# Performance work log

Hardware: AMD Instinct MI355X
Metric: run time of the kernel (lower is better)

The kernel has to match this reference:

```python
import jax, jax.numpy as jnp
import numpy as np

B, N, D = 8, 1024, 1024
H, HD = 16, 64          # n_heads, head_dim = D // H
FF = 2 * D              # SwiGLU hidden dim (ffn_dim_mult=2)
EPS = 1e-5


def setup_inputs() -> dict:
    key = jax.random.key(0)
    ks = jax.random.split(key, 10)
    s = 0.02
    return {
        "x": jax.random.normal(ks[0], (B, N, D), dtype=jnp.float32),
        "attn_norm_scale": jnp.ones((D,), jnp.float32),
        "ffn_norm_scale": jnp.ones((D,), jnp.float32),
        "wq": jax.random.normal(ks[1], (D, D), jnp.float32) * s,
        "bq": jnp.zeros((D,), jnp.float32),
        "wk": jax.random.normal(ks[2], (D, D), jnp.float32) * s,
        "bk": jnp.zeros((D,), jnp.float32),
        "wv": jax.random.normal(ks[3], (D, D), jnp.float32) * s,
        "bv": jnp.zeros((D,), jnp.float32),
        "wo": jax.random.normal(ks[4], (D, D), jnp.float32) * s,
        "bo": jnp.zeros((D,), jnp.float32),
        "w_uv": jax.random.normal(ks[5], (D, 2 * FF), jnp.float32) * s,
        "w_out": jax.random.normal(ks[6], (FF, D), jnp.float32) * s,
    }


def _rmsnorm(x, scale):
    xf = x.astype(jnp.float32)
    y = xf * jax.lax.rsqrt(jnp.mean(xf * xf, axis=-1, keepdims=True) + EPS)
    return scale * y.astype(x.dtype)


def reference(x, attn_norm_scale, ffn_norm_scale, wq, bq, wk, bk, wv, bv,
              wo, bo, w_uv, w_out):
    # FFT2D: fft over channel dim then token dim, keep real part
    x = jnp.fft.fft(jnp.fft.fft(x, axis=-1), axis=-2).real.astype(jnp.float32)

    # --- self attention with pre-RMSNorm and residual ---
    xn = _rmsnorm(x, attn_norm_scale)
    q = (xn @ wq + bq).reshape(B, N, H, HD)
    k = (xn @ wk + bk).reshape(B, N, H, HD)
    v = (xn @ wv + bv).reshape(B, N, H, HD)
    scores = jnp.einsum('bnhd,bmhd->bhnm', q, k) / np.sqrt(HD).astype(np.float32)
    attn = jax.nn.softmax(scores, axis=-1)
    o = jnp.einsum('bhnm,bmhd->bnhd', attn, v).reshape(B, N, D)
    x = (o @ wo + bo) + x

    # --- SwiGLU FFN with pre-RMSNorm and residual ---
    xn = _rmsnorm(x, ffn_norm_scale)
    uv = xn @ w_uv                      # [B, N, 2*FF]
    u, vg = uv[..., :FF], uv[..., FF:]
    x = (jax.nn.silu(u) * vg) @ w_out + x
    return x
```

## Files before the change

kernel.cpp:

```cpp
#include <hip/hip_runtime.h>
#include <stdint.h>

typedef unsigned short u16;
typedef __attribute__((ext_vector_type(8))) __bf16 bf16x8;
typedef __attribute__((ext_vector_type(4))) float f32x4;
typedef __attribute__((ext_vector_type(8))) u16 u16x8;

static __device__ __forceinline__ u16 f2bf(float f){
  uint32_t x = __builtin_bit_cast(uint32_t, f);
  x = (x + 0x7FFFu + ((x >> 16) & 1u)) >> 16;
  return (u16)x;
}
static __device__ __forceinline__ u16 f2bf_fast(float f){
  uint32_t x = __builtin_bit_cast(uint32_t, f);
  return (u16)((x + 0x8000u) >> 16);
}
static __device__ __forceinline__ float bf2f(u16 h){
  uint32_t x = ((uint32_t)h) << 16;
  return __builtin_bit_cast(float, x);
}
static __device__ __forceinline__ f32x4 mfma16(bf16x8 a, bf16x8 b, f32x4 c){
  return __builtin_amdgcn_mfma_f32_16x16x32_bf16(a, b, c, 0, 0, 0);
}
static __device__ __forceinline__ void gload16(const void* g, void* l){
  __builtin_amdgcn_global_load_lds(
      (const __attribute__((address_space(1))) void*)(uintptr_t)g,
      (__attribute__((address_space(3))) void*)(uint32_t)(uintptr_t)l,
      16, 0, 0);
}

__global__ void k_tables(u16* __restrict__ C, u16* __restrict__ S){
  int n = blockIdx.x;
  int m0 = threadIdx.x * 4;
  #pragma unroll
  for (int i = 0; i < 4; ++i){
    int m = m0 + i;
    int ph = (n * m) & 1023;
    float a = (float)ph * (1.0f / 512.0f);
    int idx = n * 1024 + m;
    C[idx] = f2bf(cospif(a)); S[idx] = f2bf(sinpif(a));
  }
}

__global__ void k_tcvt(const float* __restrict__ in, u16* __restrict__ out,
                       int R, int Cc, int64_t inB, int64_t outB){
  __shared__ float t[32][33];
  const float* ip = in + (int64_t)blockIdx.z * inB;
  u16* op = out + (int64_t)blockIdx.z * outB;
  int tc = blockIdx.x * 32, tr = blockIdx.y * 32;
  int lx = threadIdx.x & 31, ly = threadIdx.x >> 5;
  #pragma unroll
  for (int i = 0; i < 32; i += 8)
    t[ly + i][lx] = ip[(int64_t)(tr + ly + i) * Cc + tc + lx];
  __syncthreads();
  #pragma unroll
  for (int i = 0; i < 32; i += 8)
    op[(int64_t)(tc + ly + i) * R + tr + lx] = f2bf(t[lx][ly + i]);
}

__global__ void k_tcvtW(const float* __restrict__ in, u16* __restrict__ out){
  __shared__ float t[32][33];
  int tc = blockIdx.x * 32, tr = blockIdx.y * 32;
  int lx = threadIdx.x & 31, ly = threadIdx.x >> 5;
  #pragma unroll
  for (int i = 0; i < 32; i += 8)
    t[ly + i][lx] = in[(int64_t)(tr + ly + i) * 4096 + tc + lx];
  __syncthreads();
  #pragma unroll
  for (int i = 0; i < 32; i += 8){
    int c = tc + ly + i;
    int pr = (c < 2048) ? ((c >> 4) * 32 + (c & 15))
                        : (((c - 2048) >> 4) * 32 + 16 + ((c - 2048) & 15));
    out[(int64_t)pr * 1024 + tr + lx] = f2bf(t[lx][ly + i]);
  }
}

__global__ void k_bias3(const float* __restrict__ a, const float* __restrict__ b,
                        const float* __restrict__ c, float* __restrict__ o){
  int i = blockIdx.x * 256 + threadIdx.x;
  o[i] = i < 1024 ? a[i] : (i < 2048 ? b[i - 1024] : c[i - 2048]);
}

__global__ __launch_bounds__(256) void k_rmsnorm(const float* __restrict__ x,
                                                 const float* __restrict__ sc,
                                                 u16* __restrict__ out){
  int r = blockIdx.x;
  const float4* px = (const float4*)(x + (int64_t)r * 1024);
  float4 v = px[threadIdx.x];
  float ss = v.x*v.x + v.y*v.y + v.z*v.z + v.w*v.w;
  #pragma unroll
  for (int o = 1; o < 64; o <<= 1) ss += __shfl_xor(ss, o);
  __shared__ float red[4];
  if ((threadIdx.x & 63) == 0) red[threadIdx.x >> 6] = ss;
  __syncthreads();
  float tot = red[0] + red[1] + red[2] + red[3];
  float rs = rsqrtf(tot * (1.0f / 1024.0f) + 1e-5f);
  float4 s4 = ((const float4*)sc)[threadIdx.x];
  ushort4 ov;
  ov.x = f2bf(v.x * rs * s4.x); ov.y = f2bf(v.y * rs * s4.y);
  ov.z = f2bf(v.z * rs * s4.z); ov.w = f2bf(v.w * rs * s4.w);
  ((ushort4*)(out + (int64_t)r * 1024))[threadIdx.x] = ov;
}

__global__ __launch_bounds__(256) void k_fftfin(const u16* __restrict__ Uw,
                                                const float* __restrict__ sc,
                                                float* __restrict__ Y,
                                                u16* __restrict__ xn){
  int row = blockIdx.x;
  int b = row >> 10, k = row & 1023;
  int kp = (k <= 512) ? k : 1024 - k;
  float sgn = (k <= 512) ? -1.0f : 1.0f;
  const u16* ub = Uw + (int64_t)b * (1280 * 1024) + (int64_t)kp * 1024;
  const u16* wb = ub + 640 * 1024;
  int c4 = threadIdx.x * 4;
  ushort4 uu = *(const ushort4*)(ub + c4);
  ushort4 ww = *(const ushort4*)(wb + c4);
  float y0 = bf2f(uu.x) + sgn * bf2f(ww.x);
  float y1 = bf2f(uu.y) + sgn * bf2f(ww.y);
  float y2 = bf2f(uu.z) + sgn * bf2f(ww.z);
  float y3 = bf2f(uu.w) + sgn * bf2f(ww.w);
  float ss = y0*y0 + y1*y1 + y2*y2 + y3*y3;
  #pragma unroll
  for (int o = 1; o < 64; o <<= 1) ss += __shfl_xor(ss, o);
  __shared__ float red[4];
  if ((threadIdx.x & 63) == 0) red[threadIdx.x >> 6] = ss;
  __syncthreads();
  float tot = red[0] + red[1] + red[2] + red[3];
  float rs = rsqrtf(tot * (1.0f / 1024.0f) + 1e-5f);
  float4 s4 = ((const float4*)sc)[threadIdx.x];
  float4 yo; yo.x = y0; yo.y = y1; yo.z = y2; yo.w = y3;
  ((float4*)(Y + (int64_t)row * 1024))[threadIdx.x] = yo;
  ushort4 ov;
  ov.x = f2bf(y0 * rs * s4.x); ov.y = f2bf(y1 * rs * s4.y);
  ov.z = f2bf(y2 * rs * s4.z); ov.w = f2bf(y3 * rs * s4.w);
  ((ushort4*)(xn + (int64_t)row * 1024))[threadIdx.x] = ov;
}


template<int BM, bool SILU>
__global__ __launch_bounds__(512, 2) void k_gemm3(
    const u16* __restrict__ A0, const u16* __restrict__ A1,
    const u16* __restrict__ B0, const u16* __restrict__ B1,
    void* Cout, const float* __restrict__ bias, const float* resid,
    int nkt, int rowSplit, int lda, int ldb, int ldc,
    int64_t aB, int64_t bB, int64_t cB, int outBf16)
{
  constexpr int MR = BM / 32;
  constexpr int ABUF = BM * 128;
  constexpr int BBUF = 32768;
  __shared__ char smem[2 * ABUF + 2 * BBUF];
  char* Abase = smem;
  char* Bbase = smem + 2 * ABUF;

  int z = blockIdx.z;
  int nwg = gridDim.x * gridDim.y;
  int bid = blockIdx.y * gridDim.x + blockIdx.x;
  int sw = (bid & 7) * (nwg >> 3) + (bid >> 3);
  int bx = sw % gridDim.x, by = sw / gridDim.x;

  int tm = by * BM, tn = bx * 256;
  int tid = threadIdx.x;
  int lane = tid & 63, w = tid >> 6;
  int lr = lane & 15, lg = lane >> 4;
  int wOffM = (w >> 2) * (MR * 16);
  int wOffN = (w & 3) * 64;

  const u16* Ap = ((tm < rowSplit) ? A0 : A1) + (int64_t)z * aB;
  const u16* Bp = ((tm < rowSplit) ? B0 : B1) + (int64_t)z * bB;
  int64_t cOff = (int64_t)z * cB;

  int sline = tid >> 3;
  int skg8 = (((tid & 7) ^ (sline & 7)) * 8);
  int64_t aAdr = (int64_t)(tm + sline) * lda + skg8;
  int64_t bAdr = (int64_t)(tn + sline) * ldb + skg8;

  int aRB = (wOffM + lr) * 128 + ((lg ^ (lr & 7)) * 16);
  int bRB = (wOffN + lr) * 128 + ((lg ^ (lr & 7)) * 16);

  auto stA = [&](int st, int h){
    char* d = Abase + (st & 1) * ABUF + h * 16384 + tid * 16;
    const u16* s = Ap + aAdr + (int64_t)(h * 128) * lda + st * 64;
    gload16(s, d);
    gload16(s + (int64_t)64 * lda, d + 8192);
  };
  auto stB = [&](int st, int h){
    char* d = Bbase + (st & 1) * BBUF + h * 16384 + tid * 16;
    const u16* s = Bp + bAdr + (int64_t)(h * 128) * ldb + st * 64;
    gload16(s, d);
    gload16(s + (int64_t)64 * ldb, d + 8192);
  };

  const f32x4 fz = {0.f, 0.f, 0.f, 0.f};
  f32x4 acc[MR][4];
  #pragma unroll
  for (int i = 0; i < MR; ++i)
    #pragma unroll
    for (int j = 0; j < 4; ++j) acc[i][j] = fz;

  stA(0, 0); if constexpr (BM == 256) stA(0, 1);
  stB(0, 0); stB(0, 1);
  stA(1, 0); if constexpr (BM == 256) stA(1, 1);
  stB(1, 0); stB(1, 1);
  if constexpr (BM == 256) asm volatile("s_waitcnt vmcnt(8)" ::: "memory");
  else                     asm volatile("s_waitcnt vmcnt(6)" ::: "memory");
  __builtin_amdgcn_s_barrier();

  for (int kt = 0; kt < nkt; ++kt){
    const char* Ab = Abase + (kt & 1) * ABUF;
    const char* Bb = Bbase + (kt & 1) * BBUF;
    int st = kt + 2;
    bool doSt = st < nkt;
    bf16x8 bl[2][2], bh[2][2];

    if constexpr (BM == 256){
      bf16x8 al[4][2], ah[4][2];
      #pragma unroll
      for (int i = 0; i < 4; ++i)
        #pragma unroll
        for (int kc = 0; kc < 2; ++kc)
          al[i][kc] = *(const bf16x8*)(Ab + ((aRB + i * 2048) ^ (kc << 6)));
      #pragma unroll
      for (int j = 0; j < 2; ++j)
        #pragma unroll
        for (int kc = 0; kc < 2; ++kc)
          bl[j][kc] = *(const bf16x8*)(Bb + ((bRB + j * 2048) ^ (kc << 6)));
      __builtin_amdgcn_s_barrier();
      __builtin_amdgcn_s_setprio(1);
      #pragma unroll
      for (int i = 0; i < 4; ++i)
        #pragma unroll
        for (int j = 0; j < 2; ++j)
          #pragma unroll
          for (int kc = 0; kc < 2; ++kc)
            acc[i][j] = mfma16(al[i][kc], bl[j][kc], acc[i][j]);
      __builtin_amdgcn_s_setprio(0);
      __builtin_amdgcn_s_barrier();
      #pragma unroll
      for (int j = 0; j < 2; ++j)
        #pragma unroll
        for (int kc = 0; kc < 2; ++kc)
          bh[j][kc] = *(const bf16x8*)(Bb + ((bRB + (j + 2) * 2048) ^ (kc << 6)));
      if (doSt){ stA(st, 0); stB(st, 0); }
      __builtin_amdgcn_s_barrier();
      __builtin_amdgcn_s_setprio(1);
      #pragma unroll
      for (int i = 0; i < 4; ++i)
        #pragma unroll
        for (int j = 0; j < 2; ++j)
          #pragma unroll
          for (int kc = 0; kc < 2; ++kc)
            acc[i][j + 2] = mfma16(al[i][kc], bh[j][kc], acc[i][j + 2]);
      __builtin_amdgcn_s_setprio(0);
      __builtin_amdgcn_s_barrier();
      #pragma unroll
      for (int i = 0; i < 4; ++i)
        #pragma unroll
        for (int kc = 0; kc < 2; ++kc)
          ah[i][kc] = *(const bf16x8*)(Ab + ((aRB + (i + 4) * 2048) ^ (kc << 6)));
      if (doSt) stB(st, 1);
      __builtin_amdgcn_s_barrier();
      __builtin_amdgcn_s_setprio(1);
      #pragma unroll
      for (int i = 0; i < 4; ++i)
        #pragma unroll
        for (int j = 0; j < 2; ++j)
          #pragma unroll
          for (int kc = 0; kc < 2; ++kc)
            acc[i + 4][j] = mfma16(ah[i][kc], bl[j][kc], acc[i + 4][j]);
      __builtin_amdgcn_s_setprio(0);
      __builtin_amdgcn_s_barrier();
      if (doSt) stA(st, 1);
      __builtin_amdgcn_s_barrier();
      __builtin_amdgcn_s_setprio(1);
      #pragma unroll
      for (int i = 0; i < 4; ++i)
        #pragma unroll
        for (int j = 0; j < 2; ++j)
          #pragma unroll
          for (int kc = 0; kc < 2; ++kc)
            acc[i + 4][j + 2] = mfma16(ah[i][kc], bh[j][kc], acc[i + 4][j + 2]);
      __builtin_amdgcn_s_setprio(0);
      if (doSt) asm volatile("s_waitcnt vmcnt(8)" ::: "memory");
      else      asm volatile("s_waitcnt vmcnt(0)" ::: "memory");
      __builtin_amdgcn_s_barrier();
    } else {
      bf16x8 al[4][2];
      #pragma unroll
      for (int i = 0; i < 4; ++i)
        #pragma unroll
        for (int kc = 0; kc < 2; ++kc)
          al[i][kc] = *(const bf16x8*)(Ab + ((aRB + i * 2048) ^ (kc << 6)));
      #pragma unroll
      for (int j = 0; j < 2; ++j)
        #pragma unroll
        for (int kc = 0; kc < 2; ++kc)
          bl[j][kc] = *(const bf16x8*)(Bb + ((bRB + j * 2048) ^ (kc << 6)));
      __builtin_amdgcn_s_barrier();
      __builtin_amdgcn_s_setprio(1);
      #pragma unroll
      for (int i = 0; i < 4; ++i)
        #pragma unroll
        for (int j = 0; j < 2; ++j)
          #pragma unroll
          for (int kc = 0; kc < 2; ++kc)
            acc[i][j] = mfma16(al[i][kc], bl[j][kc], acc[i][j]);
      __builtin_amdgcn_s_setprio(0);
      __builtin_amdgcn_s_barrier();
      #pragma unroll
      for (int j = 0; j < 2; ++j)
        #pragma unroll
        for (int kc = 0; kc < 2; ++kc)
          bh[j][kc] = *(const bf16x8*)(Bb + ((bRB + (j + 2) * 2048) ^ (kc << 6)));
      if (doSt){ stA(st, 0); stB(st, 0); stB(st, 1); }
      __builtin_amdgcn_s_barrier();
      __builtin_amdgcn_s_setprio(1);
      #pragma unroll
      for (int i = 0; i < 4; ++i)
        #pragma unroll
        for (int j = 0; j < 2; ++j)
          #pragma unroll
          for (int kc = 0; kc < 2; ++kc)
            acc[i][j + 2] = mfma16(al[i][kc], bh[j][kc], acc[i][j + 2]);
      __builtin_amdgcn_s_setprio(0);
      if (doSt) asm volatile("s_waitcnt vmcnt(6)" ::: "memory");
      else      asm volatile("s_waitcnt vmcnt(0)" ::: "memory");
      __builtin_amdgcn_s_barrier();
    }
  }

  if constexpr (SILU){
    #pragma unroll
    for (int i = 0; i < MR; ++i){
      int colBase = ((tn + wOffN) >> 1) + lr;
      #pragma unroll
      for (int jj = 0; jj < 4; ++jj){
        int row = tm + wOffM + i * 16 + lg * 4 + jj;
        #pragma unroll
        for (int jp = 0; jp < 2; ++jp){
          float u = acc[i][jp * 2][jj], v = acc[i][jp * 2 + 1][jj];
          float s = u / (1.0f + __expf(-u));
          ((u16*)Cout)[(int64_t)row * ldc + colBase + jp * 16] = f2bf(s * v);
        }
      }
    }
  } else {
    #pragma unroll
    for (int i = 0; i < MR; ++i){
      #pragma unroll
      for (int j = 0; j < 4; ++j){
        int col = tn + wOffN + j * 16 + lr;
        float badd = bias ? bias[col] : 0.0f;
        #pragma unroll
        for (int jj = 0; jj < 4; ++jj){
          int row = tm + wOffM + i * 16 + lg * 4 + jj;
          int64_t idx = cOff + (int64_t)row * ldc + col;
          float v = acc[i][j][jj] + badd;
          if (resid) v += resid[idx];
          if (outBf16) ((u16*)Cout)[idx] = f2bf(v);
          else         ((float*)Cout)[idx] = v;
        }
      }
    }
  }
}

__global__ __launch_bounds__(256) void k_vtrans(const u16* __restrict__ qkv,
                                                u16* __restrict__ vt){
  __shared__ u16 T[64 * 65];
  int bh = blockIdx.y; int b = bh >> 4, h = bh & 15;
  int kt = blockIdx.x;
  int t = threadIdx.x;
  const u16* src = qkv + (int64_t)(b * 1024 + kt * 64) * 3072 + 2048 + h * 64;
  #pragma unroll
  for (int i = 0; i < 16; ++i){
    int idx = i * 256 + t;
    int r = idx >> 6, c = idx & 63;
    T[r * 65 + c] = src[(int64_t)r * 3072 + c];
  }
  __syncthreads();
  u16* dst = vt + (int64_t)bh * 65536 + kt * 64;
  #pragma unroll
  for (int i = 0; i < 16; ++i){
    int idx = i * 256 + t;
    int dr = idx >> 6, kc = idx & 63;
    dst[(int64_t)dr * 1024 + kc] = T[kc * 65 + dr];
  }
}

__global__ __launch_bounds__(256, 3) void k_attn2(const u16* __restrict__ qkv,
                                                  const u16* __restrict__ vt,
                                                  u16* __restrict__ O){
  __shared__ u16 Ks[2][4096];
  __shared__ u16 Vts[2][4096];
  __shared__ u16 Pl[4][2304];
  int bh = blockIdx.y; int b = bh >> 4, h = bh & 15;
  int qt = blockIdx.x;
  int t = threadIdx.x, w = t >> 6, lane = t & 63, lr = lane & 15, lg = lane >> 4;
  int sr = t >> 3, sl = t & 7;
  int swz = (sl ^ (sr & 7)) * 8;

  const u16* kg = qkv + (int64_t)b * 1024 * 3072 + 1024 + h * 64;
  const u16* vg = vt + (int64_t)bh * 65536;

  const u16* qrow = qkv + (int64_t)(b * 1024 + qt * 128 + w * 32 + lr) * 3072 + h * 64;
  bf16x8 aq[2][2];
  #pragma unroll
  for (int m = 0; m < 2; ++m)
    #pragma unroll
    for (int kc = 0; kc < 2; ++kc)
      aq[m][kc] = *(const bf16x8*)(qrow + (int64_t)m * 16 * 3072 + kc * 32 + lg * 8);

  const f32x4 fz = {0.f, 0.f, 0.f, 0.f};
  f32x4 o_[2][4];
  float lj[2][4];
  #pragma unroll
  for (int m = 0; m < 2; ++m){
    #pragma unroll
    for (int d = 0; d < 4; ++d) o_[m][d] = fz;
    #pragma unroll
    for (int j = 0; j < 4; ++j) lj[m][j] = 0.f;
  }

  #define STAGE(ktile, bn) do {                                                   \
    int r0 = sr, r1 = 32 + sr;                                                    \
    gload16(kg + (int64_t)((ktile) * 64 + r0) * 3072 + swz,                       \
            (char*)Ks + (bn) * 8192 + (t >> 6) * 1024);                           \
    gload16(kg + (int64_t)((ktile) * 64 + r1) * 3072 + swz,                       \
            (char*)Ks + (bn) * 8192 + 4096 + (t >> 6) * 1024);                    \
    gload16(vg + (int64_t)r0 * 1024 + (ktile) * 64 + swz,                         \
            (char*)Vts + (bn) * 8192 + (t >> 6) * 1024);                          \
    gload16(vg + (int64_t)r1 * 1024 + (ktile) * 64 + swz,                         \
            (char*)Vts + (bn) * 8192 + 4096 + (t >> 6) * 1024);                   \
  } while (0)

  STAGE(0, 0);
  __syncthreads();
  int buf = 0;
  int lsw = lr & 7;

  const float CSC = 0.1803368801111204f;
  const float MSH = 8.656170245333781f;

  #pragma unroll 1
  for (int kt = 0; kt < 16; ++kt){
    if (kt < 15) STAGE(kt + 1, buf ^ 1);

    f32x4 s[2][4];
    #pragma unroll
    for (int m = 0; m < 2; ++m)
      #pragma unroll
      for (int n = 0; n < 4; ++n) s[m][n] = fz;
    #pragma unroll
    for (int n = 0; n < 4; ++n){
      #pragma unroll
      for (int kc = 0; kc < 2; ++kc){
        bf16x8 kb = *(const bf16x8*)&Ks[buf][(n * 16 + lr) * 64 + (((kc * 4 + lg) ^ lsw) * 8)];
        s[0][n] = mfma16(aq[0][kc], kb, s[0][n]);
        s[1][n] = mfma16(aq[1][kc], kb, s[1][n]);
      }
    }

    #pragma unroll
    for (int m = 0; m < 2; ++m){
      #pragma unroll
      for (int j = 0; j < 4; ++j){
        float p0 = exp2f(fmaf(s[m][0][j], CSC, -MSH));
        float p1 = exp2f(fmaf(s[m][1][j], CSC, -MSH));
        float p2 = exp2f(fmaf(s[m][2][j], CSC, -MSH));
        float p3 = exp2f(fmaf(s[m][3][j], CSC, -MSH));
        lj[m][j] += (p0 + p1) + (p2 + p3);
        u16* pb = &Pl[w][(m * 16 + lg * 4 + j) * 72 + lr];
        pb[0]  = f2bf_fast(p0); pb[16] = f2bf_fast(p1);
        pb[32] = f2bf_fast(p2); pb[48] = f2bf_fast(p3);
      }
    }
    asm volatile("s_waitcnt lgkmcnt(0)" ::: "memory");
    __builtin_amdgcn_sched_barrier(0);

    #pragma unroll
    for (int kc = 0; kc < 2; ++kc){
      bf16x8 pa0 = *(const bf16x8*)&Pl[w][(lr) * 72 + kc * 32 + lg * 8];
      bf16x8 pa1 = *(const bf16x8*)&Pl[w][(16 + lr) * 72 + kc * 32 + lg * 8];
      #pragma unroll
      for (int dt = 0; dt < 4; ++dt){
        bf16x8 vb = *(const bf16x8*)&Vts[buf][(dt * 16 + lr) * 64 + (((kc * 4 + lg) ^ lsw) * 8)];
        o_[0][dt] = mfma16(pa0, vb, o_[0][dt]);
        o_[1][dt] = mfma16(pa1, vb, o_[1][dt]);
      }
    }
    __syncthreads();
    buf ^= 1;
  }
  #undef STAGE

  u16* obase = O + (int64_t)(b * 1024 + qt * 128 + w * 32) * 1024 + h * 64;
  #pragma unroll
  for (int m = 0; m < 2; ++m){
    #pragma unroll
    for (int j = 0; j < 4; ++j){
      float l = lj[m][j];
      l += __shfl_xor(l, 1); l += __shfl_xor(l, 2);
      l += __shfl_xor(l, 4); l += __shfl_xor(l, 8);
      float inv = 1.0f / l;
      int q = m * 16 + lg * 4 + j;
      #pragma unroll
      for (int dt = 0; dt < 4; ++dt)
        obase[(int64_t)q * 1024 + dt * 16 + lr] = f2bf(o_[m][dt][j] * inv);
    }
  }
}

extern "C" void kernel_launch(void* const* d_in, const int* in_sizes, int n_in,
                              void* d_out, int out_size, void* d_ws, size_t ws_size,
                              hipStream_t stream)
{
  (void)in_sizes; (void)n_in; (void)out_size; (void)ws_size;
  const float* x    = (const float*)d_in[0];
  const float* ans  = (const float*)d_in[1];
  const float* fns  = (const float*)d_in[2];
  const float* wq   = (const float*)d_in[3];
  const float* bq   = (const float*)d_in[4];
  const float* wk   = (const float*)d_in[5];
  const float* bk   = (const float*)d_in[6];
  const float* wv   = (const float*)d_in[7];
  const float* bvv  = (const float*)d_in[8];
  const float* wo   = (const float*)d_in[9];
  const float* bo   = (const float*)d_in[10];
  const float* wuv  = (const float*)d_in[11];
  const float* wout = (const float*)d_in[12];

  char* ws = (char*)d_ws;
  const size_t MB = 1u << 20;
  const int64_t M1 = 1024 * 1024;
  const int64_t FB = (int64_t)1280 * 1024;
  const int BIG = 1 << 30;
  u16*  xbt   = (u16*)(ws + 0 * MB);
  u16*  Xcs   = (u16*)(ws + 16 * MB);
  u16*  Uw    = (u16*)(ws + 36 * MB);
  u16*  xn    = (u16*)(ws + 56 * MB);
  u16*  qkv   = (u16*)(ws + 0 * MB);
  u16*  vtg   = (u16*)(ws + 72 * MB);
  u16*  Obuf  = (u16*)(ws + 88 * MB);
  u16*  xn2   = (u16*)(ws + 0 * MB);
  u16*  g     = (u16*)(ws + 16 * MB);
  u16*  Cb    = (u16*)(ws + 104 * MB);
  u16*  Sb    = (u16*)(ws + 106 * MB);
  u16*  wqkvt = (u16*)(ws + 108 * MB);
  u16*  wot   = (u16*)(ws + 114 * MB);
  u16*  wuvt  = (u16*)(ws + 116 * MB);
  u16*  woutt = (u16*)(ws + 124 * MB);
  float* bqkv = (float*)(ws + 128 * MB);
  float* outF = (float*)d_out;

  k_tables<<<dim3(1024), 256, 0, stream>>>(Cb, Sb);
  k_tcvt<<<dim3(32, 32, 8), 256, 0, stream>>>(x, xbt, 1024, 1024, M1, M1);
  k_tcvt<<<dim3(32, 32, 1), 256, 0, stream>>>(wq, wqkvt,          1024, 1024, 0, 0);
  k_tcvt<<<dim3(32, 32, 1), 256, 0, stream>>>(wk, wqkvt + M1,     1024, 1024, 0, 0);
  k_tcvt<<<dim3(32, 32, 1), 256, 0, stream>>>(wv, wqkvt + 2 * M1, 1024, 1024, 0, 0);
  k_tcvt<<<dim3(32, 32, 1), 256, 0, stream>>>(wo, wot, 1024, 1024, 0, 0);
  k_tcvtW<<<dim3(128, 32), 256, 0, stream>>>(wuv, wuvt);
  k_tcvt<<<dim3(32, 64, 1), 256, 0, stream>>>(wout, woutt, 2048, 1024, 0, 0);
  k_bias3<<<dim3(12), 256, 0, stream>>>(bq, bk, bvv, bqkv);

  k_gemm3<128,false><<<dim3(4, 10, 8), 512, 0, stream>>>(
      Cb, Sb - 640 * 1024, xbt, xbt, Xcs, nullptr, nullptr,
      16, 640, 1024, 1024, 1024, 0, M1, FB, 1);
  k_gemm3<128,false><<<dim3(4, 10, 8), 512, 0, stream>>>(
      Xcs, Xcs, Cb, Sb, Uw, nullptr, nullptr,
      16, 640, 1024, 1024, 1024, FB, 0, FB, 1);
  k_fftfin<<<dim3(8192), 256, 0, stream>>>(Uw, ans, outF, xn);

  k_gemm3<128,false><<<dim3(12, 64, 1), 512, 0, stream>>>(
      xn, xn, wqkvt, wqkvt, qkv, bqkv, nullptr,
      16, BIG, 1024, 1024, 3072, 0, 0, 0, 1);
  k_vtrans<<<dim3(16, 128), 256, 0, stream>>>(qkv, vtg);
  k_attn2<<<dim3(8, 128), 256, 0, stream>>>(qkv, vtg, Obuf);
  k_gemm3<128,false><<<dim3(4, 64, 1), 512, 0, stream>>>(
      Obuf, Obuf, wot, wot, d_out, bo, outF,
      16, BIG, 1024, 1024, 1024, 0, 0, 0, 0);

  k_rmsnorm<<<dim3(8192), 256, 0, stream>>>(outF, fns, xn2);
  k_gemm3<256,true><<<dim3(16, 32, 1), 512, 0, stream>>>(
      xn2, xn2, wuvt, wuvt, g, nullptr, nullptr,
      16, BIG, 1024, 1024, 2048, 0, 0, 0, 1);
  k_gemm3<128,false><<<dim3(4, 64, 1), 512, 0, stream>>>(
      g, g, woutt, woutt, d_out, nullptr, outF,
      32, BIG, 2048, 2048, 1024, 0, 0, 0, 0);
}
```

Baseline: 451.3 us.

## Replace large-tile GEMM with simpler 128x128 tile, BK=32 double-buffered kernel

Replaces the 512-thread GEMM, which used 128x256 or 256x256 tiles, BK=64, a two-stage prefetch and interleaved barrier/setprio phases, with a 256-thread kernel using 128x128 tiles, BK=32 and a plain double buffer. The new kernel uses 32KB of LDS, a new swizzle layout, and launch bounds allowing 4 blocks per CU, all aimed at higher occupancy and more blocks in flight. In exchange it gives up the per-block operand reuse of the larger tiles and the finer MFMA/load interleaving. It also issues a __syncthreads every K step, roughly twice as many steps as before.

Result: no change. 445.8 us (-1.2%).

```diff
diff --git a/kernel.cpp b/kernel.cpp
--- a/kernel.cpp
+++ b/kernel.cpp
@@ -136,21 +136,15 @@
   ((ushort4*)(xn + (int64_t)row * 1024))[threadIdx.x] = ov;
 }
 
-
-template<int BM, bool SILU>
-__global__ __launch_bounds__(512, 2) void k_gemm3(
+template<bool SILU>
+__global__ __launch_bounds__(256, 4) void k_gemm4(
     const u16* __restrict__ A0, const u16* __restrict__ A1,
     const u16* __restrict__ B0, const u16* __restrict__ B1,
     void* Cout, const float* __restrict__ bias, const float* resid,
     int nkt, int rowSplit, int lda, int ldb, int ldc,
     int64_t aB, int64_t bB, int64_t cB, int outBf16)
 {
-  constexpr int MR = BM / 32;
-  constexpr int ABUF = BM * 128;
-  constexpr int BBUF = 32768;
-  __shared__ char smem[2 * ABUF + 2 * BBUF];
-  char* Abase = smem;
-  char* Bbase = smem + 2 * ABUF;
+  __shared__ char smem[32768];
 
   int z = blockIdx.z;
   int nwg = gridDim.x * gridDim.y;
@@ -158,180 +152,73 @@
   int sw = (bid & 7) * (nwg >> 3) + (bid >> 3);
   int bx = sw % gridDim.x, by = sw / gridDim.x;
 
-  int tm = by * BM, tn = bx * 256;
+  int tm = by * 128, tn = bx * 128;
   int tid = threadIdx.x;
   int lane = tid & 63, w = tid >> 6;
   int lr = lane & 15, lg = lane >> 4;
-  int wOffM = (w >> 2) * (MR * 16);
-  int wOffN = (w & 3) * 64;
+  int wOffM = (w >> 1) * 64, wOffN = (w & 1) * 64;
 
   const u16* Ap = ((tm < rowSplit) ? A0 : A1) + (int64_t)z * aB;
   const u16* Bp = ((tm < rowSplit) ? B0 : B1) + (int64_t)z * bB;
   int64_t cOff = (int64_t)z * cB;
 
-  int sline = tid >> 3;
-  int skg8 = (((tid & 7) ^ (sline & 7)) * 8);
-  int64_t aAdr = (int64_t)(tm + sline) * lda + skg8;
-  int64_t bAdr = (int64_t)(tn + sline) * ldb + skg8;
-
-  int aRB = (wOffM + lr) * 128 + ((lg ^ (lr & 7)) * 16);
-  int bRB = (wOffN + lr) * 128 + ((lg ^ (lr & 7)) * 16);
-
-  auto stA = [&](int st, int h){
-    char* d = Abase + (st & 1) * ABUF + h * 16384 + tid * 16;
-    const u16* s = Ap + aAdr + (int64_t)(h * 128) * lda + st * 64;
-    gload16(s, d);
-    gload16(s + (int64_t)64 * lda, d + 8192);
+  int r0_, kg0_, r1_, kg1_;
+  {
+    int D = tid * 16, line = D >> 7, sp = ((D >> 4) & 7) ^ (line & 7);
+    r0_ = line * 2 + (sp >> 2); kg0_ = sp & 3;
+    D = tid * 16 + 4096; line = D >> 7; sp = ((D >> 4) & 7) ^ (line & 7);
+    r1_ = line * 2 + (sp >> 2); kg1_ = sp & 3;
+  }
+  int64_t aAdr0 = (int64_t)(tm + r0_) * lda + kg0_ * 8;
+  int64_t aAdr1 = (int64_t)(tm + r1_) * lda + kg1_ * 8;
+  int64_t bAdr0 = (int64_t)(tn + r0_) * ldb + kg0_ * 8;
+  int64_t bAdr1 = (int64_t)(tn + r1_) * ldb + kg1_ * 8;
+
+  int slotR = (lg + ((lr & 1) << 2)) ^ ((lr >> 1) & 7);
+  int aRB = ((wOffM >> 1) + (lr >> 1)) * 128 + slotR * 16;
+  int bRB = ((wOffN >> 1) + (lr >> 1)) * 128 + slotR * 16;
+
+  const f32x4 fz = {0.f, 0.f, 0.f, 0.f};
+  f32x4 acc[4][4];
+  #pragma unroll
+  for (int i = 0; i < 4; ++i)
+    #pragma unroll
+    for (int j = 0; j < 4; ++j) acc[i][j] = fz;
+
+  auto STAGE = [&](int kt, int bf){
+    int k0 = kt * 32;
+    char* d = smem + bf * 16384 + tid * 16;
+    gload16(Ap + aAdr0 + k0, d);
+    gload16(Ap + aAdr1 + k0, d + 4096);
+    gload16(Bp + bAdr0 + k0, d + 8192);
+    gload16(Bp + bAdr1 + k0, d + 12288);
   };
-  auto stB = [&](int st, int h){
-    char* d = Bbase + (st & 1) * BBUF + h * 16384 + tid * 16;
-    const u16* s = Bp + bAdr + (int64_t)(h * 128) * ldb + st * 64;
-    gload16(s, d);
-    gload16(s + (int64_t)64 * ldb, d + 8192);
-  };
-
-  const f32x4 fz = {0.f, 0.f, 0.f, 0.f};
-  f32x4 acc[MR][4];
-  #pragma unroll
-  for (int i = 0; i < MR; ++i)
-    #pragma unroll
-    for (int j = 0; j < 4; ++j) acc[i][j] = fz;
-
-  stA(0, 0); if constexpr (BM == 256) stA(0, 1);
-  stB(0, 0); stB(0, 1);
-  stA(1, 0); if constexpr (BM == 256) stA(1, 1);
-  stB(1, 0); stB(1, 1);
-  if constexpr (BM == 256) asm volatile("s_waitcnt vmcnt(8)" ::: "memory");
-  else                     asm volatile("s_waitcnt vmcnt(6)" ::: "memory");
-  __builtin_amdgcn_s_barrier();
-
+
+  STAGE(0, 0);
+  __syncthreads();
+  int buf = 0;
   for (int kt = 0; kt < nkt; ++kt){
-    const char* Ab = Abase + (kt & 1) * ABUF;
-    const char* Bb = Bbase + (kt & 1) * BBUF;
-    int st = kt + 2;
-    bool doSt = st < nkt;
-    bf16x8 bl[2][2], bh[2][2];
-
-    if constexpr (BM == 256){
-      bf16x8 al[4][2], ah[4][2];
-      #pragma unroll
-      for (int i = 0; i < 4; ++i)
-        #pragma unroll
-        for (int kc = 0; kc < 2; ++kc)
-          al[i][kc] = *(const bf16x8*)(Ab + ((aRB + i * 2048) ^ (kc << 6)));
-      #pragma unroll
-      for (int j = 0; j < 2; ++j)
-        #pragma unroll
-        for (int kc = 0; kc < 2; ++kc)
-          bl[j][kc] = *(const bf16x8*)(Bb + ((bRB + j * 2048) ^ (kc << 6)));
-      __builtin_amdgcn_s_barrier();
-      __builtin_amdgcn_s_setprio(1);
-      #pragma unroll
-      for (int i = 0; i < 4; ++i)
-        #pragma unroll
-        for (int j = 0; j < 2; ++j)
-          #pragma unroll
-          for (int kc = 0; kc < 2; ++kc)
-            acc[i][j] = mfma16(al[i][kc], bl[j][kc], acc[i][j]);
-      __builtin_amdgcn_s_setprio(0);
-      __builtin_amdgcn_s_barrier();
-      #pragma unroll
-      for (int j = 0; j < 2; ++j)
-        #pragma unroll
-        for (int kc = 0; kc < 2; ++kc)
-          bh[j][kc] = *(const bf16x8*)(Bb + ((bRB + (j + 2) * 2048) ^ (kc << 6)));
-      if (doSt){ stA(st, 0); stB(st, 0); }
-      __builtin_amdgcn_s_barrier();
-      __builtin_amdgcn_s_setprio(1);
-      #pragma unroll
-      for (int i = 0; i < 4; ++i)
-        #pragma unroll
-        for (int j = 0; j < 2; ++j)
-          #pragma unroll
-          for (int kc = 0; kc < 2; ++kc)
-            acc[i][j + 2] = mfma16(al[i][kc], bh[j][kc], acc[i][j + 2]);
-      __builtin_amdgcn_s_setprio(0);
-      __builtin_amdgcn_s_barrier();
-      #pragma unroll
-      for (int i = 0; i < 4; ++i)
-        #pragma unroll
-        for (int kc = 0; kc < 2; ++kc)
-          ah[i][kc] = *(const bf16x8*)(Ab + ((aRB + (i + 4) * 2048) ^ (kc << 6)));
-      if (doSt) stB(st, 1);
-      __builtin_amdgcn_s_barrier();
-      __builtin_amdgcn_s_setprio(1);
-      #pragma unroll
-      for (int i = 0; i < 4; ++i)
-        #pragma unroll
-        for (int j = 0; j < 2; ++j)
-          #pragma unroll
-          for (int kc = 0; kc < 2; ++kc)
-            acc[i + 4][j] = mfma16(ah[i][kc], bl[j][kc], acc[i + 4][j]);
-      __builtin_amdgcn_s_setprio(0);
-      __builtin_amdgcn_s_barrier();
-      if (doSt) stA(st, 1);
-      __builtin_amdgcn_s_barrier();
-      __builtin_amdgcn_s_setprio(1);
-      #pragma unroll
-      for (int i = 0; i < 4; ++i)
-        #pragma unroll
-        for (int j = 0; j < 2; ++j)
-          #pragma unroll
-          for (int kc = 0; kc < 2; ++kc)
-            acc[i + 4][j + 2] = mfma16(ah[i][kc], bh[j][kc], acc[i + 4][j + 2]);
-      __builtin_amdgcn_s_setprio(0);
-      if (doSt) asm volatile("s_waitcnt vmcnt(8)" ::: "memory");
-      else      asm volatile("s_waitcnt vmcnt(0)" ::: "memory");
-      __builtin_amdgcn_s_barrier();
-    } else {
-      bf16x8 al[4][2];
-      #pragma unroll
-      for (int i = 0; i < 4; ++i)
-        #pragma unroll
-        for (int kc = 0; kc < 2; ++kc)
-          al[i][kc] = *(const bf16x8*)(Ab + ((aRB + i * 2048) ^ (kc << 6)));
-      #pragma unroll
-      for (int j = 0; j < 2; ++j)
-        #pragma unroll
-        for (int kc = 0; kc < 2; ++kc)
-          bl[j][kc] = *(const bf16x8*)(Bb + ((bRB + j * 2048) ^ (kc << 6)));
-      __builtin_amdgcn_s_barrier();
-      __builtin_amdgcn_s_setprio(1);
-      #pragma unroll
-      for (int i = 0; i < 4; ++i)
-        #pragma unroll
-        for (int j = 0; j < 2; ++j)
-          #pragma unroll
-          for (int kc = 0; kc < 2; ++kc)
-            acc[i][j] = mfma16(al[i][kc], bl[j][kc], acc[i][j]);
-      __builtin_amdgcn_s_setprio(0);
-      __builtin_amdgcn_s_barrier();
-      #pragma unroll
-      for (int j = 0; j < 2; ++j)
-        #pragma unroll
-        for (int kc = 0; kc < 2; ++kc)
-          bh[j][kc] = *(const bf16x8*)(Bb + ((bRB + (j + 2) * 2048) ^ (kc << 6)));
-      if (doSt){ stA(st, 0); stB(st, 0); stB(st, 1); }
-      __builtin_amdgcn_s_barrier();
-      __builtin_amdgcn_s_setprio(1);
-      #pragma unroll
-      for (int i = 0; i < 4; ++i)
-        #pragma unroll
-        for (int j = 0; j < 2; ++j)
-          #pragma unroll
-          for (int kc = 0; kc < 2; ++kc)
-            acc[i][j + 2] = mfma16(al[i][kc], bh[j][kc], acc[i][j + 2]);
-      __builtin_amdgcn_s_setprio(0);
-      if (doSt) asm volatile("s_waitcnt vmcnt(6)" ::: "memory");
-      else      asm volatile("s_waitcnt vmcnt(0)" ::: "memory");
-      __builtin_amdgcn_s_barrier();
-    }
+    if (kt + 1 < nkt) STAGE(kt + 1, buf ^ 1);
+    const char* Ab = smem + buf * 16384;
+    const char* Bb = Ab + 8192;
+    bf16x8 af[4], bfr[4];
+    #pragma unroll
+    for (int i = 0; i < 4; ++i) af[i]  = *(const bf16x8*)(Ab + aRB + i * 1024);
+    #pragma unroll
+    for (int j = 0; j < 4; ++j) bfr[j] = *(const bf16x8*)(Bb + bRB + j * 1024);
+    #pragma unroll
+    for (int i = 0; i < 4; ++i)
+      #pragma unroll
+      for (int j = 0; j < 4; ++j)
+        acc[i][j] = mfma16(af[i], bfr[j], acc[i][j]);
+    __syncthreads();
+    buf ^= 1;
   }
 
   if constexpr (SILU){
-    #pragma unroll
-    for (int i = 0; i < MR; ++i){
-      int colBase = ((tn + wOffN) >> 1) + lr;
+    int colBase = ((tn + wOffN) >> 1) + lr;
+    #pragma unroll
+    for (int i = 0; i < 4; ++i){
       #pragma unroll
       for (int jj = 0; jj < 4; ++jj){
         int row = tm + wOffM + i * 16 + lg * 4 + jj;
@@ -345,7 +232,7 @@
     }
   } else {
     #pragma unroll
-    for (int i = 0; i < MR; ++i){
+    for (int i = 0; i < 4; ++i){
       #pragma unroll
       for (int j = 0; j < 4; ++j){
         int col = tn + wOffN + j * 16 + lr;
@@ -562,28 +449,28 @@
   k_tcvt<<<dim3(32, 64, 1), 256, 0, stream>>>(wout, woutt, 2048, 1024, 0, 0);
   k_bias3<<<dim3(12), 256, 0, stream>>>(bq, bk, bvv, bqkv);
 
-  k_gemm3<128,false><<<dim3(4, 10, 8), 512, 0, stream>>>(
+  k_gemm4<false><<<dim3(8, 10, 8), 256, 0, stream>>>(
       Cb, Sb - 640 * 1024, xbt, xbt, Xcs, nullptr, nullptr,
-      16, 640, 1024, 1024, 1024, 0, M1, FB, 1);
-  k_gemm3<128,false><<<dim3(4, 10, 8), 512, 0, stream>>>(
+      32, 640, 1024, 1024, 1024, 0, M1, FB, 1);
+  k_gemm4<false><<<dim3(8, 10, 8), 256, 0, stream>>>(
       Xcs, Xcs, Cb, Sb, Uw, nullptr, nullptr,
-      16, 640, 1024, 1024, 1024, FB, 0, FB, 1);
+      32, 640, 1024, 1024, 1024, FB, 0, FB, 1);
   k_fftfin<<<dim3(8192), 256, 0, stream>>>(Uw, ans, outF, xn);
 
-  k_gemm3<128,false><<<dim3(12, 64, 1), 512, 0, stream>>>(
+  k_gemm4<false><<<dim3(24, 64, 1), 256, 0, stream>>>(
       xn, xn, wqkvt, wqkvt, qkv, bqkv, nullptr,
-      16, BIG, 1024, 1024, 3072, 0, 0, 0, 1);
+      32, BIG, 1024, 1024, 3072, 0, 0, 0, 1);
   k_vtrans<<<dim3(16, 128), 256, 0, stream>>>(qkv, vtg);
   k_attn2<<<dim3(8, 128), 256, 0, stream>>>(qkv, vtg, Obuf);
-  k_gemm3<128,false><<<dim3(4, 64, 1), 512, 0, stream>>>(
+  k_gemm4<false><<<dim3(8, 64, 1), 256, 0, stream>>>(
       Obuf, Obuf, wot, wot, d_out, bo, outF,
-      16, BIG, 1024, 1024, 1024, 0, 0, 0, 0);
+      32, BIG, 1024, 1024, 1024, 0, 0, 0, 0);
 
   k_rmsnorm<<<dim3(8192), 256, 0, stream>>>(outF, fns, xn2);
-  k_gemm3<256,true><<<dim3(16, 32, 1), 512, 0, stream>>>(
+  k_gemm4<true><<<dim3(32, 64, 1), 256, 0, stream>>>(
       xn2, xn2, wuvt, wuvt, g, nullptr, nullptr,
-      16, BIG, 1024, 1024, 2048, 0, 0, 0, 1);
-  k_gemm3<128,false><<<dim3(4, 64, 1), 512, 0, stream>>>(
+      32, BIG, 1024, 1024, 2048, 0, 0, 0, 1);
+  k_gemm4<false><<<dim3(8, 64, 1), 256, 0, stream>>>(
       g, g, woutt, woutt, d_out, nullptr, outF,
-      32, BIG, 2048, 2048, 1024, 0, 0, 0, 0);
-}
+      64, BIG, 2048, 2048, 1024, 0, 0, 0, 0);
+}
```
